# Optimization experiments

Hardware: AMD Instinct MI355X
Metric: run time of the kernel (lower is better)

## Reference

```python
import jax, jax.numpy as jnp
import numpy as np

N = 50000
E = 100000
D = 768


def setup_inputs() -> dict:
    key = jax.random.key(0)
    ks = jax.random.split(key, 8)
    x = jax.random.normal(ks[0], (N, D), dtype=jnp.float32)
    edge_index = jax.random.randint(ks[1], (2, E), 0, N, dtype=jnp.int64)
    s = 1.0 / np.sqrt(D)
    W1l = jax.random.uniform(ks[2], (D, D), jnp.float32, -s, s)
    b1l = jax.random.uniform(ks[3], (D,), jnp.float32, -s, s)
    W1r = jax.random.uniform(ks[4], (D, D), jnp.float32, -s, s)
    W2l = jax.random.uniform(ks[5], (D, D), jnp.float32, -s, s)
    b2l = jax.random.uniform(ks[6], (D,), jnp.float32, -s, s)
    W2r = jax.random.uniform(ks[7], (D, D), jnp.float32, -s, s)
    return {"x": x, "edge_index": edge_index, "W1l": W1l, "b1l": b1l,
            "W1r": W1r, "W2l": W2l, "b2l": b2l, "W2r": W2r}


def sage_conv(x, src, dst, Wl, bl, Wr):
    # mean-aggregate neighbor (source) features at target nodes
    summed = jax.ops.segment_sum(x[src], dst, num_segments=N)  # [N, D]
    deg = jax.ops.segment_sum(jnp.ones((src.shape[0],), x.dtype), dst,
                              num_segments=N)
    agg = summed / jnp.clip(deg, 1.0)[:, None]
    # lin_l(agg) + lin_r(x)  (PyG SAGEConv: lin_l has bias, lin_r does not)
    return agg @ Wl.T + bl + x @ Wr.T


def reference(x, edge_index, W1l, b1l, W1r, W2l, b2l, W2r):
    src, dst = edge_index[0], edge_index[1]
    h = sage_conv(x, src, dst, W1l, b1l, W1r)
    h = jax.nn.relu(h)
    return sage_conv(h, src, dst, W2l, b2l, W2r)
```

## Files before the change

kernel.cpp:

```cpp
#include <hip/hip_runtime.h>
#include <stdint.h>

#define NN 50000
#define NE 100000
#define DD 768
#define KC 1536
#define SCAN_B 196

typedef __attribute__((ext_vector_type(8))) __bf16 bf16x8;
typedef __attribute__((ext_vector_type(4))) float floatx4;

static __device__ __forceinline__ float bf2f(unsigned short u) {
    union { unsigned int u; float f; } c; c.u = ((unsigned int)u) << 16; return c.f;
}
static __device__ __forceinline__ unsigned short f2bf(float f) {
    union { float f; unsigned int u; } c; c.f = f;
    return (unsigned short)((c.u + 0x7FFFu + ((c.u >> 16) & 1u)) >> 16);
}

static __device__ __forceinline__ void gld16(const void* g, void* l) {
    __builtin_amdgcn_global_load_lds(
        (const __attribute__((address_space(1))) unsigned int*)g,
        (__attribute__((address_space(3))) unsigned int*)l, 16, 0, 0);
}


__global__ __launch_bounds__(192) void k_convert_x(const float* __restrict__ x,
                                                   unsigned short* __restrict__ acat) {
    const int n = blockIdx.x;
    const int c = threadIdx.x * 4;
    const float4 v = *(const float4*)(x + (size_t)n * DD + c);
    ushort4 o;
    o.x = f2bf(v.x); o.y = f2bf(v.y); o.z = f2bf(v.z); o.w = f2bf(v.w);
    *(ushort4*)(acat + (size_t)n * KC + DD + c) = o;
}

__global__ __launch_bounds__(384) void k_convert_w(const float* __restrict__ W1l,
                                                   const float* __restrict__ W1r,
                                                   const float* __restrict__ W2l,
                                                   const float* __restrict__ W2r,
                                                   unsigned short* __restrict__ B1,
                                                   unsigned short* __restrict__ B2) {
    const int j = blockIdx.x;
    const int layer = blockIdx.y;
    const int k = threadIdx.x * 4;
    const float* Wl = layer ? W2l : W1l;
    const float* Wr = layer ? W2r : W1r;
    unsigned short* B = layer ? B2 : B1;
    const float4 v = (k < DD) ? *(const float4*)(Wl + (size_t)j * DD + k)
                              : *(const float4*)(Wr + (size_t)j * DD + (k - DD));
    ushort4 o; o.x = f2bf(v.x); o.y = f2bf(v.y); o.z = f2bf(v.z); o.w = f2bf(v.w);
    *(ushort4*)(B + (size_t)j * KC + k) = o;
}


__global__ __launch_bounds__(256) void k_hist(const int* __restrict__ dst,
                                              int* __restrict__ cnt) {
    int e = blockIdx.x * 256 + threadIdx.x;
    if (e < NE) atomicAdd(&cnt[dst[e]], 1);
}

__global__ __launch_bounds__(256) void k_scan1(const int* __restrict__ cnt,
                                               int* __restrict__ rowptr,
                                               int* __restrict__ partial) {
    __shared__ int buf[256];
    const int t = threadIdx.x;
    const int i = blockIdx.x * 256 + t;
    int v = (i < NN) ? cnt[i] : 0;
    buf[t] = v;
    __syncthreads();
#pragma unroll
    for (int off = 1; off < 256; off <<= 1) {
        int u = (t >= off) ? buf[t - off] : 0;
        __syncthreads();
        buf[t] += u;
        __syncthreads();
    }
    if (i < NN) rowptr[i + 1] = buf[t];
    if (t == 255) partial[blockIdx.x] = buf[255];
}

__global__ __launch_bounds__(256) void k_scan2(int* __restrict__ partial) {
    __shared__ int buf[256];
    const int t = threadIdx.x;
    int v = (t < SCAN_B) ? partial[t] : 0;
    buf[t] = v;
    __syncthreads();
#pragma unroll
    for (int off = 1; off < 256; off <<= 1) {
        int u = (t >= off) ? buf[t - off] : 0;
        __syncthreads();
        buf[t] += u;
        __syncthreads();
    }
    if (t < SCAN_B) partial[t] = buf[t] - v;
}

__global__ __launch_bounds__(256) void k_scan3(int* __restrict__ rowptr,
                                               const int* __restrict__ partial) {
    const int i = blockIdx.x * 256 + threadIdx.x;
    if (i < NN) rowptr[i + 1] += partial[blockIdx.x];
    if (i == 0) rowptr[0] = 0;
}

__global__ __launch_bounds__(256) void k_fill(const int* __restrict__ src,
                                              const int* __restrict__ dst,
                                              const int* __restrict__ rowptr,
                                              int* __restrict__ cursor,
                                              int* __restrict__ esrc) {
    int e = blockIdx.x * 256 + threadIdx.x;
    if (e < NE) {
        const int d = dst[e];
        const int pos = atomicAdd(&cursor[d], 1);
        esrc[rowptr[d] + pos] = src[e];
    }
}

__global__ __launch_bounds__(192) void k_agg(const unsigned short* __restrict__ srcmat,
                                             const int* __restrict__ rowptr,
                                             const int* __restrict__ esrc,
                                             unsigned short* __restrict__ dstmat) {
    const int n = blockIdx.x;
    const int c = threadIdx.x * 4;
    const int beg = rowptr[n], end = rowptr[n + 1];
    float4 a = {0.f, 0.f, 0.f, 0.f};
    for (int e = beg; e < end; ++e) {
        const int s = esrc[e];
        const ushort4 v = *(const ushort4*)(srcmat + (size_t)s * KC + DD + c);
        a.x += bf2f(v.x); a.y += bf2f(v.y); a.z += bf2f(v.z); a.w += bf2f(v.w);
    }
    const float inv = (end > beg) ? 1.0f / (float)(end - beg) : 1.0f;
    ushort4 o;
    o.x = f2bf(a.x * inv); o.y = f2bf(a.y * inv);
    o.z = f2bf(a.z * inv); o.w = f2bf(a.w * inv);
    *(ushort4*)(dstmat + (size_t)n * KC + c) = o;
}

template <int MODE>
__global__ __launch_bounds__(256) void k_gemm(const unsigned short* __restrict__ A,
                                              const unsigned short* __restrict__ B,
                                              const float* __restrict__ bias,
                                              unsigned short* __restrict__ outA,
                                              float* __restrict__ outF) {
    __shared__ alignas(16) unsigned short sA[128 * 32];
    __shared__ alignas(16) unsigned short sB[128 * 32];
    const int tid = threadIdx.x;
    const int w = tid >> 6, lane = tid & 63;
    const int quad = lane >> 4, r16 = lane & 15;
    const int wm = (w & 1) * 64, wn = (w >> 1) * 64;
    const int tm = blockIdx.x, tn = blockIdx.y;
    const int rowBase = tm * 128;

    floatx4 acc[4][4];
#pragma unroll
    for (int i = 0; i < 4; ++i)
#pragma unroll
        for (int j = 0; j < 4; ++j) acc[i][j] = (floatx4){0.f, 0.f, 0.f, 0.f};

    for (int kt = 0; kt < KC / 32; ++kt) {
        const int k0 = kt * 32;
#pragma unroll
        for (int q = 0; q < 2; ++q) {
            const int c0 = (w * 2 + q) * 64;
            const int c = c0 + lane;
            const int row = c >> 2;
            const int col = (c & 3) * 8;
            int gr = rowBase + row; if (gr > NN - 1) gr = NN - 1;
            gld16(A + (size_t)gr * KC + k0 + col, sA + (size_t)c0 * 8);
            gld16(B + (size_t)(tn * 128 + row) * KC + k0 + col, sB + (size_t)c0 * 8);
        }
        __syncthreads();
        bf16x8 af[4], bfr[4];
#pragma unroll
        for (int i = 0; i < 4; ++i)
            af[i] = *(const bf16x8*)(sA + (wm + i * 16 + r16) * 32 + quad * 8);
#pragma unroll
        for (int j = 0; j < 4; ++j)
            bfr[j] = *(const bf16x8*)(sB + (wn + j * 16 + r16) * 32 + quad * 8);
#pragma unroll
        for (int i = 0; i < 4; ++i)
#pragma unroll
            for (int j = 0; j < 4; ++j)
                acc[i][j] = __builtin_amdgcn_mfma_f32_16x16x32_bf16(af[i], bfr[j], acc[i][j], 0, 0, 0);
        __syncthreads();
    }

#pragma unroll
    for (int i = 0; i < 4; ++i)
#pragma unroll
        for (int j = 0; j < 4; ++j) {
            const int gcol = tn * 128 + wn + j * 16 + r16;
            const float bv = bias[gcol];
#pragma unroll
            for (int rr = 0; rr < 4; ++rr) {
                const int grow = rowBase + wm + i * 16 + quad * 4 + rr;
                if (grow < NN) {
                    float v = acc[i][j][rr] + bv;
                    if (MODE == 0) {
                        v = fmaxf(v, 0.0f);
                        outA[(size_t)grow * KC + DD + gcol] = f2bf(v);
                    } else {
                        outF[(size_t)grow * DD + gcol] = v;
                    }
                }
            }
        }
}

extern "C" void kernel_launch(void* const* d_in, const int* in_sizes, int n_in,
                              void* d_out, int out_size, void* d_ws, size_t ws_size,
                              hipStream_t stream) {
    const float* x   = (const float*)d_in[0];
    const int*   ei  = (const int*)d_in[1];
    const float* W1l = (const float*)d_in[2];
    const float* b1l = (const float*)d_in[3];
    const float* W1r = (const float*)d_in[4];
    const float* W2l = (const float*)d_in[5];
    const float* b2l = (const float*)d_in[6];
    const float* W2r = (const float*)d_in[7];
    const int* src = ei;
    const int* dst = ei + NE;
    float* out = (float*)d_out;

    char* ws = (char*)d_ws;
    unsigned short* Acat1 = (unsigned short*)ws;
    unsigned short* Acat2 = (unsigned short*)(ws + (size_t)NN * KC * 2);
    unsigned short* B1    = (unsigned short*)(ws + (size_t)NN * KC * 4);
    unsigned short* B2    = B1 + (size_t)DD * KC;
    int* cnt    = (int*)(ws + (size_t)NN * KC * 4 + (size_t)DD * KC * 4);
    int* rowptr = cnt + NN;
    int* esrc   = rowptr + NN + 1;
    int* partial = esrc + NE;

    hipMemsetAsync(cnt, 0, NN * sizeof(int), stream);
    k_hist<<<(NE + 255) / 256, 256, 0, stream>>>(dst, cnt);
    k_scan1<<<SCAN_B, 256, 0, stream>>>(cnt, rowptr, partial);
    k_scan2<<<1, 256, 0, stream>>>(partial);
    k_scan3<<<SCAN_B, 256, 0, stream>>>(rowptr, partial);
    hipMemsetAsync(cnt, 0, NN * sizeof(int), stream);
    k_fill<<<(NE + 255) / 256, 256, 0, stream>>>(src, dst, rowptr, cnt, esrc);

    k_convert_x<<<NN, 192, 0, stream>>>(x, Acat1);
    dim3 wgrid(DD, 2);
    k_convert_w<<<wgrid, 384, 0, stream>>>(W1l, W1r, W2l, W2r, B1, B2);

    dim3 ggrid((NN + 127) / 128, DD / 128);

    k_agg<<<NN, 192, 0, stream>>>(Acat1, rowptr, esrc, Acat1);
    k_gemm<0><<<ggrid, 256, 0, stream>>>(Acat1, B1, b1l, Acat2, nullptr);

    k_agg<<<NN, 192, 0, stream>>>(Acat2, rowptr, esrc, Acat2);
    k_gemm<1><<<ggrid, 256, 0, stream>>>(Acat2, B2, b2l, nullptr, out);
}
```

Measured before the change: 774.2 us.

## Double-buffer GEMM LDS tiles and remap workgroups for XCD-aware locality

The GEMM kernel now uses two LDS buffers so the next K-tile's global-to-LDS loads are issued before the MFMA work on the current tile, removing one barrier per iteration and overlapping load latency with compute. The 2D grid becomes a 1D grid with a remapping that hands contiguous tile ranges to each of the 8 XCDs, so the 6 column tiles sharing one row block of A run on the same XCD and reuse its L2. LDS use per block doubles, which may lower occupancy.

```diff
diff --git a/kernel.cpp b/kernel.cpp
--- a/kernel.cpp
+++ b/kernel.cpp
@@ -6,6 +6,8 @@
 #define DD 768
 #define KC 1536
 #define SCAN_B 196
+#define NTM 391
+#define NTN 6
 
 typedef __attribute__((ext_vector_type(8))) __bf16 bf16x8;
 typedef __attribute__((ext_vector_type(4))) float floatx4;
@@ -142,13 +144,19 @@
                                               const float* __restrict__ bias,
                                               unsigned short* __restrict__ outA,
                                               float* __restrict__ outF) {
-    __shared__ alignas(16) unsigned short sA[128 * 32];
-    __shared__ alignas(16) unsigned short sB[128 * 32];
+    __shared__ alignas(16) unsigned short sA[2][128 * 32];
+    __shared__ alignas(16) unsigned short sB[2][128 * 32];
     const int tid = threadIdx.x;
     const int w = tid >> 6, lane = tid & 63;
     const int quad = lane >> 4, r16 = lane & 15;
     const int wm = (w & 1) * 64, wn = (w >> 1) * 64;
-    const int tm = blockIdx.x, tn = blockIdx.y;
+
+    const int nwg = NTM * NTN;
+    const int q = nwg >> 3, r = nwg & 7;
+    const int xcd = blockIdx.x & 7, slot = blockIdx.x >> 3;
+    const int L = (xcd < r ? xcd * (q + 1) : r * (q + 1) + (xcd - r) * q) + slot;
+    const int tn = L % NTN;
+    const int tm = L / NTN;
     const int rowBase = tm * 128;
 
     floatx4 acc[4][4];
@@ -157,32 +165,41 @@
 #pragma unroll
         for (int j = 0; j < 4; ++j) acc[i][j] = (floatx4){0.f, 0.f, 0.f, 0.f};
 
-    for (int kt = 0; kt < KC / 32; ++kt) {
+    auto stage = [&](int buf, int kt) {
         const int k0 = kt * 32;
 #pragma unroll
-        for (int q = 0; q < 2; ++q) {
-            const int c0 = (w * 2 + q) * 64;
+        for (int qq = 0; qq < 2; ++qq) {
+            const int c0 = (w * 2 + qq) * 64;
             const int c = c0 + lane;
             const int row = c >> 2;
             const int col = (c & 3) * 8;
             int gr = rowBase + row; if (gr > NN - 1) gr = NN - 1;
-            gld16(A + (size_t)gr * KC + k0 + col, sA + (size_t)c0 * 8);
-            gld16(B + (size_t)(tn * 128 + row) * KC + k0 + col, sB + (size_t)c0 * 8);
+            gld16(A + (size_t)gr * KC + k0 + col, &sA[buf][(size_t)c0 * 8]);
+            gld16(B + (size_t)(tn * 128 + row) * KC + k0 + col, &sB[buf][(size_t)c0 * 8]);
         }
-        __syncthreads();
+    };
+
+    const int nk = KC / 32;
+    int cur = 0;
+    stage(0, 0);
+    __syncthreads();
+
+    for (int kt = 0; kt < nk; ++kt) {
+        if (kt + 1 < nk) stage(cur ^ 1, kt + 1);
         bf16x8 af[4], bfr[4];
 #pragma unroll
         for (int i = 0; i < 4; ++i)
-            af[i] = *(const bf16x8*)(sA + (wm + i * 16 + r16) * 32 + quad * 8);
+            af[i] = *(const bf16x8*)(&sA[cur][(wm + i * 16 + r16) * 32 + quad * 8]);
 #pragma unroll
         for (int j = 0; j < 4; ++j)
-            bfr[j] = *(const bf16x8*)(sB + (wn + j * 16 + r16) * 32 + quad * 8);
+            bfr[j] = *(const bf16x8*)(&sB[cur][(wn + j * 16 + r16) * 32 + quad * 8]);
 #pragma unroll
         for (int i = 0; i < 4; ++i)
 #pragma unroll
             for (int j = 0; j < 4; ++j)
                 acc[i][j] = __builtin_amdgcn_mfma_f32_16x16x32_bf16(af[i], bfr[j], acc[i][j], 0, 0, 0);
         __syncthreads();
+        cur ^= 1;
     }
 
 #pragma unroll
@@ -244,7 +261,7 @@
     dim3 wgrid(DD, 2);
     k_convert_w<<<wgrid, 384, 0, stream>>>(W1l, W1r, W2l, W2r, B1, B2);
 
-    dim3 ggrid((NN + 127) / 128, DD / 128);
+    const int ggrid = NTM * NTN;
 
     k_agg<<<NN, 192, 0, stream>>>(Acat1, rowptr, esrc, Acat1);
     k_gemm<0><<<ggrid, 256, 0, stream>>>(Acat1, B1, b1l, Acat2, nullptr);
```

New measurement: 773.5 us. Within noise of the previous version (-0.1%).
